# Performance work log

Hardware: AMD Instinct MI355X
Metric: run time of the kernel (lower is better)

Reference implementation:

```python
import jax, jax.numpy as jnp
import numpy as np

B, C, T, F = 2, 256, 1024, 64
N, HID = 4, 64


def setup_inputs() -> dict:
    key = jax.random.key(0)
    ks = jax.random.split(key, 9)
    s = 0.02
    return {
        "x": jax.random.normal(ks[0], (B, C, T, F), dtype=jnp.float32),
        "Wq": jax.random.normal(ks[1], (N, HID, C), dtype=jnp.float32) * s,
        "bq": jnp.zeros((N, HID), dtype=jnp.float32),
        "Wk": jax.random.normal(ks[2], (N, HID, C), dtype=jnp.float32) * s,
        "bk": jnp.zeros((N, HID), dtype=jnp.float32),
        "Wv": jax.random.normal(ks[3], (N, C // N, C), dtype=jnp.float32) * s,
        "bv": jnp.zeros((N, C // N), dtype=jnp.float32),
        "Wp": jax.random.normal(ks[4], (C, C), dtype=jnp.float32) * s,
        "bp": jnp.zeros((C,), dtype=jnp.float32),
    }


def reference(x, Wq, bq, Wk, bk, Wv, bv, Wp, bp):
    b, c, t, f = x.shape
    n = Wq.shape[0]
    # conv1x1 per head then torch: cat(dim=0) -> [N*b, h, t, f]; transpose(1,2); flatten -> [N*b, t, h*f]
    def proj(W, bias):
        h = W.shape[1]
        y = jnp.einsum('bctf,nhc->nbthf', x, W) + bias[:, None, None, :, None]
        return y.reshape(n * b, t, h * f)

    Q = proj(Wq, bq)                       # [N*b, t, hid*f]
    K = proj(Wk, bk)                       # [N*b, t, hid*f]
    V = proj(Wv, bv)                       # [N*b, t, (c/N)*f]

    scale = 1.0 / jnp.sqrt(jnp.asarray(Q.shape[-1], dtype=x.dtype))
    attn = jax.nn.softmax(jnp.einsum('mte,mse->mts', Q, K) * scale, axis=2)
    Vo = jnp.einsum('mts,msd->mtd', attn, V)             # [N*b, t, c*f/N]

    # torch: reshape(b*N, t, c*f//N).transpose(1,2).view(N,b,c//N,t,f).transpose(0,1).view(b,c,t,f)
    Vo = Vo.transpose(0, 2, 1)                            # [N*b, c*f/N, t]
    Vo = Vo.reshape(n, b, c // n, t, f)
    Vo = jnp.swapaxes(Vo, 0, 1).reshape(b, c, t, f)

    out = jnp.einsum('bctf,oc->botf', Vo, Wp) + bp[None, :, None, None]
    return out + x
```

## Files before the change

### kernel.cpp

```cpp
#include <hip/hip_runtime.h>

#define DI __device__ __forceinline__

static constexpr int B_ = 2;
static constexpr int C_ = 256;
static constexpr int T_ = 1024;
static constexpr int F_ = 64;
static constexpr int M_ = 8;
static constexpr int E_ = 4096;
static constexpr float SCALE_ = 1.0f / 64.0f;

typedef __attribute__((ext_vector_type(8))) short bf16x8;
typedef __attribute__((ext_vector_type(4))) float f32x4;

DI unsigned short bf16_rne(float f) {
    unsigned int u = __float_as_uint(f);
    return (unsigned short)((u + 0x7FFFu + ((u >> 16) & 1u)) >> 16);
}
DI float bf2f(unsigned short h) { return __uint_as_float(((unsigned int)h) << 16); }
DI ushort4 pack4(float a, float b, float c, float d) {
    return make_ushort4(bf16_rne(a), bf16_rne(b), bf16_rne(c), bf16_rne(d));
}
DI float4 up4(ushort4 u) {
    return make_float4(bf2f(u.x), bf2f(u.y), bf2f(u.z), bf2f(u.w));
}

DI void gload_lds16(const unsigned short* g, unsigned short* l) {
    __builtin_amdgcn_global_load_lds(
        (const __attribute__((address_space(1))) unsigned int*)g,
        (__attribute__((address_space(3))) unsigned int*)l, 16, 0, 0);
}

DI void mfma16(f32x4& acc, bf16x8 a, bf16x8 b) {
    asm("v_mfma_f32_16x16x32_bf16 %0, %1, %2, %0" : "+v"(acc) : "v"(a), "v"(b));
}

__global__ __launch_bounds__(256) void wconv_kernel(
    const float* __restrict__ Wq, const float* __restrict__ Wk,
    const float* __restrict__ Wv, const float* __restrict__ Wp,
    const float* __restrict__ bq, const float* __restrict__ bk,
    const float* __restrict__ bv,
    unsigned short* __restrict__ Wall, unsigned short* __restrict__ Wpb,
    float* __restrict__ bias_all)
{
    const int tid = (int)threadIdx.x;
    const int bid = (int)blockIdx.x;
    if (bid < 192) {
        const int idx = (bid * 256 + tid) * 4;
        const int proj = idx >> 16, rem = idx & 65535;
        const float* src = proj == 0 ? Wq : (proj == 1 ? Wk : Wv);
        float4 v = *(const float4*)(src + rem);
        *(ushort4*)(Wall + idx) = pack4(v.x, v.y, v.z, v.w);
        const int gid = bid * 256 + tid;
        if (gid < 768) {
            float bb = gid < 256 ? bq[gid] : (gid < 512 ? bk[gid - 256] : bv[gid - 512]);
            bias_all[gid] = bb;
        }
    } else {
        const int idx = ((bid - 192) * 256 + tid) * 4;
        float4 v = *(const float4*)(Wp + idx);
        *(ushort4*)(Wpb + idx) = pack4(v.x, v.y, v.z, v.w);
    }
}

__global__ __launch_bounds__(256) void qkv_one(
    const float* __restrict__ x, const unsigned short* __restrict__ Wall,
    const float* __restrict__ bias_all, unsigned short* __restrict__ outQ)
{
    const int wgid = (int)blockIdx.x;
    const int b = wgid >> 9, tft = wgid & 511;
    const int tfbase = tft * 128;

    const int tid = (int)threadIdx.x;
    const int wid = tid >> 6, lane = tid & 63;
    const int wr = wid >> 1, wc = wid & 1;
    const int lo16 = lane & 15, hi4 = lane >> 4;

    __shared__ unsigned short As[4 * 128 * 64];
    __shared__ unsigned short Bs[128 * 64];

    {
        const int a = lane & 7, cg = lane >> 3;
        const int rowb = wid * 32 + a * 4;
        const float* xb = x + (size_t)b * (C_ * T_ * F_) + tfbase + rowb;
        for (int cb = 0; cb < 256; cb += 64) {
            const int c0 = cb + cg * 8;
            float4 v[8];
#pragma unroll
            for (int g = 0; g < 8; ++g)
                v[g] = *(const float4*)(xb + (size_t)(c0 + g) * 65536);
            const int kc = cb >> 6;
#pragma unroll
            for (int j = 0; j < 4; ++j) {
                const int row = rowb + j;
                const int col8 = cg ^ (row & 7);
                float e0 = (&v[0].x)[j], e1 = (&v[1].x)[j], e2 = (&v[2].x)[j], e3 = (&v[3].x)[j];
                float e4 = (&v[4].x)[j], e5 = (&v[5].x)[j], e6 = (&v[6].x)[j], e7 = (&v[7].x)[j];
                ushort4 p0 = pack4(e0, e1, e2, e3);
                ushort4 p1 = pack4(e4, e5, e6, e7);
                *(ushort4*)&As[kc * 8192 + row * 64 + col8 * 8]     = p0;
                *(ushort4*)&As[kc * 8192 + row * 64 + col8 * 8 + 4] = p1;
            }
        }
    }

    const int srow = lane >> 3;
    const int scol = ((lane & 7) ^ srow) * 8;
    const int tf0 = tfbase + wr * 64;

    const int krot = wgid & 3;
    int nrot = wgid % 6;

    __syncthreads();

    for (int ntl_i = 0; ntl_i < 6; ++ntl_i) {
        int ntl = ntl_i + nrot; if (ntl >= 6) ntl -= 6;
        const int nbase = ntl * 128;
        const unsigned short* brow = Wall + (size_t)nbase * 256;
        f32x4 acc[4][4] = {};

        for (int kc_i = 0; kc_i < 4; ++kc_i) {
            const int kc = (kc_i + krot) & 3;
#pragma unroll
            for (int i = 0; i < 4; ++i) {
                const int rb = wid * 32 + i * 8;
                gload_lds16(brow + (size_t)(rb + srow) * 256 + kc * 64 + scol,
                            &Bs[rb * 64]);
            }
            __syncthreads();
#pragma unroll
            for (int kk = 0; kk < 2; ++kk) {
                const int hc = (kk * 32 + hi4 * 8) ^ ((lane & 7) << 3);
                bf16x8 a[4], bb[4];
#pragma unroll
                for (int mi = 0; mi < 4; ++mi)
                    a[mi] = *(const bf16x8*)&As[kc * 8192 + (wr * 64 + mi * 16 + lo16) * 64 + hc];
#pragma unroll
                for (int nj = 0; nj < 4; ++nj)
                    bb[nj] = *(const bf16x8*)&Bs[(wc * 64 + nj * 16 + lo16) * 64 + hc];
#pragma unroll
                for (int mi = 0; mi < 4; ++mi)
#pragma unroll
                    for (int nj = 0; nj < 4; ++nj)
                        mfma16(acc[mi][nj], a[mi], bb[nj]);
            }
            __syncthreads();
        }

        asm volatile("s_nop 7\n\ts_nop 7" ::: "memory");
#pragma unroll
        for (int nj = 0; nj < 4; ++nj) {
            const int r_col = nbase + wc * 64 + nj * 16 + lo16;
            const int projl = r_col >> 8;
            const int rr = r_col & 255;
            const int mrow = (rr >> 6) * 2 + b;
            const int h = rr & 63;
            const float bv = bias_all[r_col];
            unsigned short* dst0 = outQ + (size_t)projl * 33554432
                                 + (size_t)mrow * (T_ * E_) + h * 64;
#pragma unroll
            for (int mi = 0; mi < 4; ++mi) {
                const int tf = tf0 + mi * 16 + hi4 * 4;
                const int t = tf >> 6, f = tf & 63;
                *(ushort4*)(dst0 + (size_t)t * E_ + f) =
                    pack4(acc[mi][nj][0] + bv, acc[mi][nj][1] + bv,
                          acc[mi][nj][2] + bv, acc[mi][nj][3] + bv);
            }
        }
        if (ntl_i < 5) __syncthreads();
    }
}

__global__ __launch_bounds__(256) void scores_mfma(
    const unsigned short* __restrict__ Q, const unsigned short* __restrict__ K,
    unsigned short* __restrict__ S)
{
    const int orig = (int)blockIdx.x;
    const int wg = (orig & 7) * 64 + (orig >> 3);
    const int m = wg >> 6;
    const int rest = wg & 63;
    const int sbase = (rest & 7) * 128;
    const int tbase = (rest >> 3) * 128;
    const int tid = (int)threadIdx.x;
    const int wid = tid >> 6, lane = tid & 63;
    const int wr = wid >> 1, wc = wid & 1;
    const int lo16 = lane & 15, hi4 = lane >> 4;

    __shared__ unsigned short As[128 * 64];
    __shared__ unsigned short Bs[128 * 64];

    f32x4 acc[4][4] = {};

    const unsigned short* qrow = Q + ((size_t)m * T_ + tbase) * E_;
    const unsigned short* krow = K + ((size_t)m * T_ + sbase) * E_;

    const int srow = lane >> 3;
    const int scol = ((lane & 7) ^ srow) * 8;

    for (int eb = 0; eb < E_; eb += 64) {
#pragma unroll
        for (int i = 0; i < 4; ++i) {
            const int rb = wid * 32 + i * 8;
            gload_lds16(qrow + (size_t)(rb + srow) * E_ + eb + scol, &As[rb * 64]);
            gload_lds16(krow + (size_t)(rb + srow) * E_ + eb + scol, &Bs[rb * 64]);
        }
        __syncthreads();
#pragma unroll
        for (int kk = 0; kk < 2; ++kk) {
            const int hc = (kk * 32 + hi4 * 8) ^ ((lane & 7) << 3);
            bf16x8 a[4], bb[4];
#pragma unroll
            for (int mi = 0; mi < 4; ++mi)
                a[mi] = *(const bf16x8*)&As[(wr * 64 + mi * 16 + lo16) * 64 + hc];
#pragma unroll
            for (int nj = 0; nj < 4; ++nj)
                bb[nj] = *(const bf16x8*)&Bs[(wc * 64 + nj * 16 + lo16) * 64 + hc];
#pragma unroll
            for (int mi = 0; mi < 4; ++mi)
#pragma unroll
                for (int nj = 0; nj < 4; ++nj)
                    mfma16(acc[mi][nj], a[mi], bb[nj]);
        }
        __syncthreads();
    }

    asm volatile("s_nop 7\n\ts_nop 7" ::: "memory");
#pragma unroll
    for (int mi = 0; mi < 4; ++mi)
#pragma unroll
        for (int r = 0; r < 4; ++r) {
            int trow = tbase + wr * 64 + mi * 16 + hi4 * 4 + r;
            unsigned short* sp = S + ((size_t)m * T_ + trow) * T_ + sbase + wc * 64 + lo16;
#pragma unroll
            for (int nj = 0; nj < 4; ++nj)
                sp[nj * 16] = bf16_rne(acc[mi][nj][r] * SCALE_);
        }
}

__global__ __launch_bounds__(256) void softmax_kernel(
    const unsigned short* __restrict__ S, unsigned short* __restrict__ A)
{
    const int tid = (int)threadIdx.x;
    const int wid = tid >> 6, lane = tid & 63;
    const size_t rowoff = ((size_t)blockIdx.x * 4 + wid) * 1024;

    const size_t off = rowoff + lane * 16;
    bf16x8 u0 = *(const bf16x8*)(S + off);
    bf16x8 u1 = *(const bf16x8*)(S + off + 8);

    float v[16];
#pragma unroll
    for (int i = 0; i < 8; ++i) {
        v[i]     = bf2f((unsigned short)u0[i]);
        v[i + 8] = bf2f((unsigned short)u1[i]);
    }

    float mx = v[0];
#pragma unroll
    for (int i = 1; i < 16; ++i) mx = fmaxf(mx, v[i]);
#pragma unroll
    for (int off2 = 32; off2 > 0; off2 >>= 1) mx = fmaxf(mx, __shfl_xor(mx, off2));

    float sm = 0.f;
#pragma unroll
    for (int i = 0; i < 16; ++i) { v[i] = __expf(v[i] - mx); sm += v[i]; }
#pragma unroll
    for (int off2 = 32; off2 > 0; off2 >>= 1) sm += __shfl_xor(sm, off2);
    const float inv = 1.0f / sm;

    bf16x8 r0, r1;
#pragma unroll
    for (int i = 0; i < 8; ++i) {
        r0[i] = (short)bf16_rne(v[i] * inv);
        r1[i] = (short)bf16_rne(v[i + 8] * inv);
    }
    *(bf16x8*)(A + off)     = r0;
    *(bf16x8*)(A + off + 8) = r1;
}

__global__ __launch_bounds__(256) void vt_kernel(
    const unsigned short* __restrict__ V, unsigned short* __restrict__ Vt)
{
    const int m = blockIdx.z;
    const int d0 = blockIdx.x * 64;
    const int s0 = blockIdx.y * 64;
    const int tid = (int)threadIdx.x;
    __shared__ unsigned short ts[64][68];

    const unsigned short* vp = V + (size_t)m * T_ * E_;
#pragma unroll
    for (int it = 0; it < 4; ++it) {
        int idx = it * 256 + tid;
        int sl = idx >> 4, d4 = (idx & 15) * 4;
        *(ushort4*)&ts[sl][d4] = *(const ushort4*)&vp[(size_t)(s0 + sl) * E_ + d0 + d4];
    }
    __syncthreads();
    unsigned short* op = Vt + (size_t)m * E_ * T_;
    const int dl = tid >> 2, s16 = (tid & 3) * 16;
#pragma unroll
    for (int q = 0; q < 4; ++q) {
        int s4 = s16 + q * 4;
        ushort4 v = make_ushort4(ts[s4][dl], ts[s4+1][dl], ts[s4+2][dl], ts[s4+3][dl]);
        *(ushort4*)&op[(size_t)(d0 + dl) * T_ + s0 + s4] = v;
    }
}

__global__ __launch_bounds__(256) void pv_mfma(
    const unsigned short* __restrict__ A, const unsigned short* __restrict__ Vt,
    unsigned short* __restrict__ G)
{
    const int orig = (int)blockIdx.x;
    const int wg = (orig & 7) * 256 + (orig >> 3);
    const int m = wg >> 8;
    const int rest = wg & 255;
    const int dbase = (rest & 31) * 128;
    const int tbase = (rest >> 5) * 128;
    const int nh = m >> 1, b = m & 1;
    const int tid = (int)threadIdx.x;
    const int wid = tid >> 6, lane = tid & 63;
    const int wr = wid >> 1, wc = wid & 1;
    const int lo16 = lane & 15, hi4 = lane >> 4;

    __shared__ unsigned short As[128 * 64];
    __shared__ unsigned short Bs[128 * 64];

    f32x4 acc[4][4] = {};

    const unsigned short* arow = A  + ((size_t)m * T_ + tbase) * T_;
    const unsigned short* vrow = Vt + (size_t)m * E_ * T_ + (size_t)dbase * T_;

    const int srow = lane >> 3;
    const int scol = ((lane & 7) ^ srow) * 8;

    for (int sb = 0; sb < T_; sb += 64) {
#pragma unroll
        for (int i = 0; i < 4; ++i) {
            const int rb = wid * 32 + i * 8;
            gload_lds16(arow + (size_t)(rb + srow) * T_ + sb + scol, &As[rb * 64]);
            gload_lds16(vrow + (size_t)(rb + srow) * T_ + sb + scol, &Bs[rb * 64]);
        }
        __syncthreads();
#pragma unroll
        for (int kk = 0; kk < 2; ++kk) {
            const int hc = (kk * 32 + hi4 * 8) ^ ((lane & 7) << 3);
            bf16x8 a[4], bb[4];
#pragma unroll
            for (int mi = 0; mi < 4; ++mi)
                a[mi] = *(const bf16x8*)&As[(wr * 64 + mi * 16 + lo16) * 64 + hc];
#pragma unroll
            for (int nj = 0; nj < 4; ++nj)
                bb[nj] = *(const bf16x8*)&Bs[(wc * 64 + nj * 16 + lo16) * 64 + hc];
#pragma unroll
            for (int mi = 0; mi < 4; ++mi)
#pragma unroll
                for (int nj = 0; nj < 4; ++nj)
                    mfma16(acc[mi][nj], a[mi], bb[nj]);
        }
        __syncthreads();
    }

    asm volatile("s_nop 7\n\ts_nop 7" ::: "memory");
    const int cb   = nh * 64 + (dbase >> 6) + wc;
    const int t2lo = (tbase >> 6) + wr;
#pragma unroll
    for (int mi = 0; mi < 4; ++mi) {
        const int tl = mi * 16 + hi4 * 4;
#pragma unroll
        for (int nj = 0; nj < 4; ++nj) {
            const int d63 = nj * 16 + lo16;
            size_t addr = (((size_t)(b * 256 + cb)) * 1024 + d63 * 16 + t2lo) * 64 + tl;
            *(ushort4*)&G[addr] = pack4(acc[mi][nj][0], acc[mi][nj][1],
                                        acc[mi][nj][2], acc[mi][nj][3]);
        }
    }
}

__global__ __launch_bounds__(256) void outproj_fused(
    const unsigned short* __restrict__ G, const unsigned short* __restrict__ Wpb,
    const float* __restrict__ bp, const float* __restrict__ x,
    float* __restrict__ out)
{
    const int tfbase = blockIdx.x * 128;
    const int obase  = blockIdx.y * 128;
    const int b      = blockIdx.z;
    const int tid = (int)threadIdx.x;
    const int wid = tid >> 6, lane = tid & 63;
    const int wr = wid >> 1, wc = wid & 1;
    const int lo16 = lane & 15, hi4 = lane >> 4;

    __shared__ unsigned short As[128 * 64];
    __shared__ unsigned short Bs[128 * 64];

    f32x4 acc[4][4] = {};

    const unsigned short* brow = Wpb + (size_t)obase * 256;

    const int srow = lane >> 3;
    const int scol = ((lane & 7) ^ srow) * 8;

    const int cg = tid >> 4;
    const int ag = tid & 15;

    for (int cb = 0; cb < 256; cb += 64) {
#pragma unroll
        for (int i = 0; i < 4; ++i) {
            const int rb = wid * 32 + i * 8;
            gload_lds16(brow + (size_t)(rb + srow) * 256 + cb + scol, &Bs[rb * 64]);
        }
        {
            const unsigned short* gb = G + ((size_t)(b * 256 + cb + cg * 4)) * 65536
                                     + tfbase + ag * 8;
            bf16x8 vv0 = *(const bf16x8*)(gb);
            bf16x8 vv1 = *(const bf16x8*)(gb + 65536);
            bf16x8 vv2 = *(const bf16x8*)(gb + 2 * 65536);
            bf16x8 vv3 = *(const bf16x8*)(gb + 3 * 65536);
#pragma unroll
            for (int j = 0; j < 8; ++j) {
                const int row = ag * 8 + j;
                const int phys = row * 64 + ((((cg >> 1) ^ (row & 7)) << 3) + (cg & 1) * 4);
                ushort4 w = make_ushort4((unsigned short)vv0[j], (unsigned short)vv1[j],
                                         (unsigned short)vv2[j], (unsigned short)vv3[j]);
                *(ushort4*)&As[phys] = w;
            }
        }
        __syncthreads();
#pragma unroll
        for (int kk = 0; kk < 2; ++kk) {
            const int hc = (kk * 32 + hi4 * 8) ^ ((lane & 7) << 3);
            bf16x8 a[4], bb[4];
#pragma unroll
            for (int mi = 0; mi < 4; ++mi)
                a[mi] = *(const bf16x8*)&As[(wr * 64 + mi * 16 + lo16) * 64 + hc];
#pragma unroll
            for (int nj = 0; nj < 4; ++nj)
                bb[nj] = *(const bf16x8*)&Bs[(wc * 64 + nj * 16 + lo16) * 64 + hc];
#pragma unroll
            for (int mi = 0; mi < 4; ++mi)
#pragma unroll
                for (int nj = 0; nj < 4; ++nj)
                    mfma16(acc[mi][nj], a[mi], bb[nj]);
        }
        __syncthreads();
    }

    asm volatile("s_nop 7\n\ts_nop 7" ::: "memory");
#pragma unroll
    for (int nj = 0; nj < 4; ++nj) {
        const int o = obase + wc * 64 + nj * 16 + lo16;
        const float bias = bp[o];
        const size_t rowb = ((size_t)(b * 256 + o)) * 65536;
#pragma unroll
        for (int mi = 0; mi < 4; ++mi) {
            const int tf = tfbase + wr * 64 + mi * 16 + hi4 * 4;
            float4 xv = *(const float4*)(x + rowb + tf);
            float4 r = make_float4(acc[mi][nj][0] + bias + xv.x,
                                   acc[mi][nj][1] + bias + xv.y,
                                   acc[mi][nj][2] + bias + xv.z,
                                   acc[mi][nj][3] + bias + xv.w);
            *(float4*)(out + rowb + tf) = r;
        }
    }
}

extern "C" void kernel_launch(void* const* d_in, const int* in_sizes, int n_in,
                              void* d_out, int out_size, void* d_ws, size_t ws_size,
                              hipStream_t stream) {
    const float* x  = (const float*)d_in[0];
    const float* Wq = (const float*)d_in[1];
    const float* bq = (const float*)d_in[2];
    const float* Wk = (const float*)d_in[3];
    const float* bk = (const float*)d_in[4];
    const float* Wv = (const float*)d_in[5];
    const float* bv = (const float*)d_in[6];
    const float* Wp = (const float*)d_in[7];
    const float* bp = (const float*)d_in[8];
    float* out = (float*)d_out;

    char* ws = (char*)d_ws;
    unsigned short* Q    = (unsigned short*)(ws);
    unsigned short* K    = (unsigned short*)(ws + 67108864);
    unsigned short* V    = (unsigned short*)(ws + 134217728);
    unsigned short* S    = (unsigned short*)(ws + 201326592);
    unsigned short* A    = (unsigned short*)(ws + 218103808);
    unsigned short* Wall = (unsigned short*)(ws + 234881024);
    float* bias_all      = (float*)(ws + 235274240);
    unsigned short* Wpb  = (unsigned short*)(ws + 235277312);
    unsigned short* Vt = K;
    unsigned short* G  = Q;

    wconv_kernel<<<256, 256, 0, stream>>>(Wq, Wk, Wv, Wp, bq, bk, bv, Wall, Wpb, bias_all);
    qkv_one<<<1024, 256, 0, stream>>>(x, Wall, bias_all, Q);
    scores_mfma<<<512, 256, 0, stream>>>(Q, K, S);
    softmax_kernel<<<2048, 256, 0, stream>>>(S, A);
    vt_kernel<<<dim3(64, 16, M_), 256, 0, stream>>>(V, Vt);
    pv_mfma<<<2048, 256, 0, stream>>>(A, Vt, G);
    outproj_fused<<<dim3(512, 2, 2), 256, 0, stream>>>(G, Wpb, bp, x, out);
}
```

Measured before the change: 396.3 us.

## Enlarge PV GEMM tiles to 256x256 with double-buffered LDS prefetch

Replaces the 128x128 PV kernel with a 256x256 tile, 512-thread (8-wave) version that double-buffers A and Vt tiles in LDS and prefetches the next K slice before computing the current one. It uses waitcnt, raw barriers and setprio to overlap global-to-LDS loads with MFMA work. Larger tiles improve data reuse per load. The costs are 128KB of LDS per block, which limits occupancy, and a grid of only 512 blocks, which may leave compute units underused.

Result: no change. 398.1 us (+0.5%).

```diff
diff --git a/kernel.cpp b/kernel.cpp
--- a/kernel.cpp
+++ b/kernel.cpp
@@ -305,70 +305,90 @@
     }
 }
 
-__global__ __launch_bounds__(256) void pv_mfma(
+__global__ __launch_bounds__(512) void pv_256(
     const unsigned short* __restrict__ A, const unsigned short* __restrict__ Vt,
     unsigned short* __restrict__ G)
 {
     const int orig = (int)blockIdx.x;
-    const int wg = (orig & 7) * 256 + (orig >> 3);
-    const int m = wg >> 8;
-    const int rest = wg & 255;
-    const int dbase = (rest & 31) * 128;
-    const int tbase = (rest >> 5) * 128;
+    const int wg = (orig & 7) * 64 + (orig >> 3);
+    const int m = wg >> 6;
+    const int rest = wg & 63;
+    const int dbase = (rest & 15) * 256;
+    const int tbase = (rest >> 4) * 256;
     const int nh = m >> 1, b = m & 1;
+
     const int tid = (int)threadIdx.x;
     const int wid = tid >> 6, lane = tid & 63;
-    const int wr = wid >> 1, wc = wid & 1;
+    const int wr = wid >> 2, wc = wid & 3;
     const int lo16 = lane & 15, hi4 = lane >> 4;
 
-    __shared__ unsigned short As[128 * 64];
-    __shared__ unsigned short Bs[128 * 64];
-
-    f32x4 acc[4][4] = {};
+    __shared__ unsigned short As[2][256 * 64];
+    __shared__ unsigned short Bs[2][256 * 64];
+
+    f32x4 acc[8][4] = {};
 
     const unsigned short* arow = A  + ((size_t)m * T_ + tbase) * T_;
     const unsigned short* vrow = Vt + (size_t)m * E_ * T_ + (size_t)dbase * T_;
 
-    const int srow = lane >> 3;
-    const int scol = ((lane & 7) ^ srow) * 8;
-
-    for (int sb = 0; sb < T_; sb += 64) {
-#pragma unroll
-        for (int i = 0; i < 4; ++i) {
-            const int rb = wid * 32 + i * 8;
-            gload_lds16(arow + (size_t)(rb + srow) * T_ + sb + scol, &As[rb * 64]);
-            gload_lds16(vrow + (size_t)(rb + srow) * T_ + sb + scol, &Bs[rb * 64]);
-        }
-        __syncthreads();
+    const int srowL = lane >> 3;
+    const int scolL = ((lane & 7) ^ srowL) * 8;
+
+#define PV_STAGE(buf, sb)                                                     \
+    _Pragma("unroll")                                                         \
+    for (int r_ = 0; r_ < 4; ++r_) {                                          \
+        const int rb_ = r_ * 64 + wid * 8;                                    \
+        gload_lds16(arow + (size_t)(rb_ + srowL) * T_ + (sb) + scolL,         \
+                    &As[buf][rb_ * 64]);                                      \
+        gload_lds16(vrow + (size_t)(rb_ + srowL) * T_ + (sb) + scolL,         \
+                    &Bs[buf][rb_ * 64]);                                      \
+    }
+
+    PV_STAGE(0, 0);
+
+#pragma unroll 1
+    for (int k = 0; k < 16; ++k) {
+        const int cur = k & 1;
+        if (k < 15) {
+            PV_STAGE(cur ^ 1, (k + 1) * 64);
+            asm volatile("s_waitcnt vmcnt(8)" ::: "memory");
+        } else {
+            asm volatile("s_waitcnt vmcnt(0)" ::: "memory");
+        }
+        __builtin_amdgcn_s_barrier();
+        __builtin_amdgcn_sched_barrier(0);
+
+        __builtin_amdgcn_s_setprio(1);
 #pragma unroll
         for (int kk = 0; kk < 2; ++kk) {
             const int hc = (kk * 32 + hi4 * 8) ^ ((lane & 7) << 3);
-            bf16x8 a[4], bb[4];
-#pragma unroll
-            for (int mi = 0; mi < 4; ++mi)
-                a[mi] = *(const bf16x8*)&As[(wr * 64 + mi * 16 + lo16) * 64 + hc];
+            bf16x8 af[8], bf[4];
+#pragma unroll
+            for (int mi = 0; mi < 8; ++mi)
+                af[mi] = *(const bf16x8*)&As[cur][(wr * 128 + mi * 16 + lo16) * 64 + hc];
 #pragma unroll
             for (int nj = 0; nj < 4; ++nj)
-                bb[nj] = *(const bf16x8*)&Bs[(wc * 64 + nj * 16 + lo16) * 64 + hc];
-#pragma unroll
-            for (int mi = 0; mi < 4; ++mi)
+                bf[nj] = *(const bf16x8*)&Bs[cur][(wc * 64 + nj * 16 + lo16) * 64 + hc];
+#pragma unroll
+            for (int mi = 0; mi < 8; ++mi)
 #pragma unroll
                 for (int nj = 0; nj < 4; ++nj)
-                    mfma16(acc[mi][nj], a[mi], bb[nj]);
-        }
-        __syncthreads();
-    }
+                    mfma16(acc[mi][nj], af[mi], bf[nj]);
+        }
+        __builtin_amdgcn_s_setprio(0);
+        __builtin_amdgcn_s_barrier();
+    }
+#undef PV_STAGE
 
     asm volatile("s_nop 7\n\ts_nop 7" ::: "memory");
-    const int cb   = nh * 64 + (dbase >> 6) + wc;
-    const int t2lo = (tbase >> 6) + wr;
-#pragma unroll
-    for (int mi = 0; mi < 4; ++mi) {
-        const int tl = mi * 16 + hi4 * 4;
+    const int c = nh * 64 + (dbase >> 6) + wc;
+#pragma unroll
+    for (int mi = 0; mi < 8; ++mi) {
+        const int t = tbase + wr * 128 + mi * 16 + hi4 * 4;
+        const int t_hi = t >> 6, t_lo = t & 63;
 #pragma unroll
         for (int nj = 0; nj < 4; ++nj) {
             const int d63 = nj * 16 + lo16;
-            size_t addr = (((size_t)(b * 256 + cb)) * 1024 + d63 * 16 + t2lo) * 64 + tl;
+            size_t addr = (((size_t)(b * 256 + c)) * 1024 + d63 * 16 + t_hi) * 64 + t_lo;
             *(ushort4*)&G[addr] = pack4(acc[mi][nj][0], acc[mi][nj][1],
                                         acc[mi][nj][2], acc[mi][nj][3]);
         }
@@ -493,6 +513,6 @@
     scores_mfma<<<512, 256, 0, stream>>>(Q, K, S);
     softmax_kernel<<<2048, 256, 0, stream>>>(S, A);
     vt_kernel<<<dim3(64, 16, M_), 256, 0, stream>>>(V, Vt);
-    pv_mfma<<<2048, 256, 0, stream>>>(A, Vt, G);
+    pv_256<<<512, 512, 0, stream>>>(A, Vt, G);
     outproj_fused<<<dim3(512, 2, 2), 256, 0, stream>>>(G, Wpb, bp, x, out);
 }
```

## Halve QKV projection M-tile and double-buffer weight tiles with async prefetch

Applied to the files above, without the earlier changes.

The QKV projection kernel now uses 64-row tiles instead of 128, doubling the grid to 2048 workgroups and cutting LDS for the activation tile. Weight tiles are double-buffered: the next K-chunk is prefetched with direct-to-LDS loads while the current one feeds MFMAs, using vmcnt waits and raw barriers in place of __syncthreads. The x staging loop is software-pipelined with a register prefetch, and the wave priority is raised around the MFMA block. In exchange, weights are reloaded twice as often per output row, the per-workgroup rotation of tile and K-chunk order is dropped, and MFMA reuse per A fragment falls.

Result: slower. 417.5 us (+5.3%).

```diff
diff --git a/kernel.cpp b/kernel.cpp
--- a/kernel.cpp
+++ b/kernel.cpp
@@ -63,91 +63,115 @@
     }
 }
 
-__global__ __launch_bounds__(256) void qkv_one(
+__global__ __launch_bounds__(256) void qkv_six(
     const float* __restrict__ x, const unsigned short* __restrict__ Wall,
     const float* __restrict__ bias_all, unsigned short* __restrict__ outQ)
 {
     const int wgid = (int)blockIdx.x;
-    const int b = wgid >> 9, tft = wgid & 511;
-    const int tfbase = tft * 128;
+    const int b = wgid >> 10, tft = wgid & 1023;
+    const int tfbase = tft * 64;
 
     const int tid = (int)threadIdx.x;
     const int wid = tid >> 6, lane = tid & 63;
     const int wr = wid >> 1, wc = wid & 1;
     const int lo16 = lane & 15, hi4 = lane >> 4;
 
-    __shared__ unsigned short As[4 * 128 * 64];
-    __shared__ unsigned short Bs[128 * 64];
+    __shared__ unsigned short As[4 * 64 * 64];
+    __shared__ unsigned short Bs[2][128 * 64];
+
+    const int srow = lane >> 3;
+    const int scol = ((lane & 7) ^ srow) * 8;
+
+#pragma unroll
+    for (int i = 0; i < 4; ++i) {
+        const int rb = wid * 32 + i * 8;
+        gload_lds16(Wall + (size_t)(rb + srow) * 256 + scol, &Bs[0][rb * 64]);
+    }
 
     {
-        const int a = lane & 7, cg = lane >> 3;
-        const int rowb = wid * 32 + a * 4;
+        const int a = lane & 3, cg = lane >> 2;
+        const int rowb = wid * 16 + a * 4;
         const float* xb = x + (size_t)b * (C_ * T_ * F_) + tfbase + rowb;
-        for (int cb = 0; cb < 256; cb += 64) {
-            const int c0 = cb + cg * 8;
-            float4 v[8];
-#pragma unroll
-            for (int g = 0; g < 8; ++g)
-                v[g] = *(const float4*)(xb + (size_t)(c0 + g) * 65536);
-            const int kc = cb >> 6;
+        const size_t cstep = 65536;
+
+        float4 va[4], vb[4];
+#pragma unroll
+        for (int g = 0; g < 4; ++g)
+            va[g] = *(const float4*)(xb + (size_t)(cg * 4 + g) * cstep);
+
+#pragma unroll
+        for (int cb = 0; cb < 4; ++cb) {
+            if (cb < 3) {
+                const int c0n = (cb + 1) * 64 + cg * 4;
+#pragma unroll
+                for (int g = 0; g < 4; ++g)
+                    vb[g] = *(const float4*)(xb + (size_t)(c0n + g) * cstep);
+            }
 #pragma unroll
             for (int j = 0; j < 4; ++j) {
                 const int row = rowb + j;
-                const int col8 = cg ^ (row & 7);
-                float e0 = (&v[0].x)[j], e1 = (&v[1].x)[j], e2 = (&v[2].x)[j], e3 = (&v[3].x)[j];
-                float e4 = (&v[4].x)[j], e5 = (&v[5].x)[j], e6 = (&v[6].x)[j], e7 = (&v[7].x)[j];
-                ushort4 p0 = pack4(e0, e1, e2, e3);
-                ushort4 p1 = pack4(e4, e5, e6, e7);
-                *(ushort4*)&As[kc * 8192 + row * 64 + col8 * 8]     = p0;
-                *(ushort4*)&As[kc * 8192 + row * 64 + col8 * 8 + 4] = p1;
+                const int phys = row * 64 + (((cg >> 1) ^ (row & 7)) << 3) + (cg & 1) * 4;
+                float e0 = (&va[0].x)[j], e1 = (&va[1].x)[j];
+                float e2 = (&va[2].x)[j], e3 = (&va[3].x)[j];
+                *(ushort4*)&As[cb * 4096 + phys] = pack4(e0, e1, e2, e3);
             }
-        }
-    }
-
-    const int srow = lane >> 3;
-    const int scol = ((lane & 7) ^ srow) * 8;
-    const int tf0 = tfbase + wr * 64;
-
-    const int krot = wgid & 3;
-    int nrot = wgid % 6;
+#pragma unroll
+            for (int g = 0; g < 4; ++g) va[g] = vb[g];
+        }
+    }
 
     __syncthreads();
 
-    for (int ntl_i = 0; ntl_i < 6; ++ntl_i) {
-        int ntl = ntl_i + nrot; if (ntl >= 6) ntl -= 6;
-        const int nbase = ntl * 128;
-        const unsigned short* brow = Wall + (size_t)nbase * 256;
-        f32x4 acc[4][4] = {};
-
-        for (int kc_i = 0; kc_i < 4; ++kc_i) {
-            const int kc = (kc_i + krot) & 3;
-#pragma unroll
-            for (int i = 0; i < 4; ++i) {
-                const int rb = wid * 32 + i * 8;
-                gload_lds16(brow + (size_t)(rb + srow) * 256 + kc * 64 + scol,
-                            &Bs[rb * 64]);
+    const int tf0 = tfbase + wr * 32;
+
+#pragma unroll 1
+    for (int ntl = 0; ntl < 6; ++ntl) {
+        f32x4 acc[2][4] = {};
+
+#pragma unroll
+        for (int kc = 0; kc < 4; ++kc) {
+            const int nk = ntl * 4 + kc;
+            const int cur = nk & 1;
+            if (nk < 23) {
+                const int nn = nk + 1;
+                const unsigned short* bsrc =
+                    Wall + (size_t)(nn >> 2) * 32768 + (size_t)(nn & 3) * 64;
+#pragma unroll
+                for (int i = 0; i < 4; ++i) {
+                    const int rb = wid * 32 + i * 8;
+                    gload_lds16(bsrc + (size_t)(rb + srow) * 256 + scol,
+                                &Bs[cur ^ 1][rb * 64]);
+                }
+                asm volatile("s_waitcnt vmcnt(4)" ::: "memory");
+            } else {
+                asm volatile("s_waitcnt vmcnt(0)" ::: "memory");
             }
-            __syncthreads();
+            __builtin_amdgcn_s_barrier();
+            __builtin_amdgcn_sched_barrier(0);
+
+            __builtin_amdgcn_s_setprio(1);
 #pragma unroll
             for (int kk = 0; kk < 2; ++kk) {
                 const int hc = (kk * 32 + hi4 * 8) ^ ((lane & 7) << 3);
-                bf16x8 a[4], bb[4];
-#pragma unroll
-                for (int mi = 0; mi < 4; ++mi)
-                    a[mi] = *(const bf16x8*)&As[kc * 8192 + (wr * 64 + mi * 16 + lo16) * 64 + hc];
+                bf16x8 a[2], bb[4];
+#pragma unroll
+                for (int mi = 0; mi < 2; ++mi)
+                    a[mi] = *(const bf16x8*)&As[kc * 4096 + (wr * 32 + mi * 16 + lo16) * 64 + hc];
 #pragma unroll
                 for (int nj = 0; nj < 4; ++nj)
-                    bb[nj] = *(const bf16x8*)&Bs[(wc * 64 + nj * 16 + lo16) * 64 + hc];
-#pragma unroll
-                for (int mi = 0; mi < 4; ++mi)
+                    bb[nj] = *(const bf16x8*)&Bs[cur][(wc * 64 + nj * 16 + lo16) * 64 + hc];
+#pragma unroll
+                for (int mi = 0; mi < 2; ++mi)
 #pragma unroll
                     for (int nj = 0; nj < 4; ++nj)
                         mfma16(acc[mi][nj], a[mi], bb[nj]);
             }
-            __syncthreads();
+            __builtin_amdgcn_s_setprio(0);
+            __builtin_amdgcn_s_barrier();
         }
 
         asm volatile("s_nop 7\n\ts_nop 7" ::: "memory");
+        const int nbase = ntl * 128;
 #pragma unroll
         for (int nj = 0; nj < 4; ++nj) {
             const int r_col = nbase + wc * 64 + nj * 16 + lo16;
@@ -159,7 +183,7 @@
             unsigned short* dst0 = outQ + (size_t)projl * 33554432
                                  + (size_t)mrow * (T_ * E_) + h * 64;
 #pragma unroll
-            for (int mi = 0; mi < 4; ++mi) {
+            for (int mi = 0; mi < 2; ++mi) {
                 const int tf = tf0 + mi * 16 + hi4 * 4;
                 const int t = tf >> 6, f = tf & 63;
                 *(ushort4*)(dst0 + (size_t)t * E_ + f) =
@@ -167,7 +191,6 @@
                           acc[mi][nj][2] + bv, acc[mi][nj][3] + bv);
             }
         }
-        if (ntl_i < 5) __syncthreads();
     }
 }
 
@@ -489,7 +512,7 @@
     unsigned short* G  = Q;
 
     wconv_kernel<<<256, 256, 0, stream>>>(Wq, Wk, Wv, Wp, bq, bk, bv, Wall, Wpb, bias_all);
-    qkv_one<<<1024, 256, 0, stream>>>(x, Wall, bias_all, Q);
+    qkv_six<<<2048, 256, 0, stream>>>(x, Wall, bias_all, Q);
     scores_mfma<<<512, 256, 0, stream>>>(Q, K, S);
     softmax_kernel<<<2048, 256, 0, stream>>>(S, A);
     vt_kernel<<<dim3(64, 16, M_), 256, 0, stream>>>(V, Vt);
```
